# Kernel tuning notes

Measured on AMD Instinct MI355X. Metric: run time of the kernel, lower is better.

Reference implementation:

```python
import jax, jax.numpy as jnp
import numpy as np

NODE_CNT = 1_000_000
EMBED_DIM = 64
B = 4096
N0, N1 = 10, 25          # neighbor_cnt_list = [10, 25]
H0, H1 = 128, 128        # hidden_dim_list = [128, 128]


def setup_inputs() -> dict:
    key = jax.random.key(0)
    k_in, k_n0, k_n1, k_emb, k_w1, k_w0, k_b0 = jax.random.split(key, 7)
    inputs = jax.random.randint(k_in, (B,), 0, NODE_CNT, dtype=jnp.int32)
    neigh0 = jax.random.randint(k_n0, (B, N0), 0, NODE_CNT, dtype=jnp.int32)
    neigh1 = jax.random.randint(k_n1, (B, N0, N1), 0, NODE_CNT, dtype=jnp.int32)
    # learned parameters
    embed_table = jax.random.normal(k_emb, (NODE_CNT + 1, EMBED_DIM), dtype=jnp.float32) * 0.05
    # fc1: deepest layer, linear, no bias: (embed + mean-agg embed) -> H1
    W1 = jax.random.normal(k_w1, (2 * EMBED_DIM, H1), dtype=jnp.float32) * (1.0 / np.sqrt(2 * EMBED_DIM))
    # fc0: output layer, sigmoid + bias: (embed + mean-agg h1) -> H0
    W0 = jax.random.normal(k_w0, (EMBED_DIM + H1, H0), dtype=jnp.float32) * (1.0 / np.sqrt(EMBED_DIM + H1))
    b0 = jnp.zeros((H0,), dtype=jnp.float32)
    return {"inputs": inputs, "neigh0": neigh0, "neigh1": neigh1,
            "embed_table": embed_table, "W1": W1, "W0": W0, "b0": b0}


def reference(inputs, neigh0, neigh1, embed_table, W1, W0, b0):
    # ---- deepest level (k = 1): raw embedding gather + mean aggregate ----
    e_nn = embed_table[neigh1]                    # [B, N0, N1, D] irregular gather
    agg1 = jnp.mean(e_nn, axis=2)                 # [B, N0, D]
    e_n = embed_table[neigh0]                     # [B, N0, D]
    # fc1: linear, no bias, no activation
    h1 = jnp.concatenate([e_n, agg1], axis=-1) @ W1   # [B, N0, H1]
    # ---- level k = 0: aggregate layer-1 vectors of sampled neighbors ----
    agg0 = jnp.mean(h1, axis=1)                   # [B, H1]
    e_v = embed_table[inputs]                     # [B, D]
    # fc0: dense with bias + sigmoid
    h0 = jax.nn.sigmoid(jnp.concatenate([e_v, agg0], axis=-1) @ W0 + b0)  # [B, H0]
    return h0
```

## Files before the change

kernel.cpp:

```cpp
#include <hip/hip_runtime.h>
#include <math.h>


constexpr int D   = 64;
constexpr int N0  = 10;
constexpr int N1  = 25;
constexpr int NN  = N0 * N1;
constexpr int H1  = 128;
constexpr int H0  = 128;
constexpr int K0  = D + H1;
constexpr int BPB = 2;
constexpr int NT  = 256;

__global__ __launch_bounds__(NT, 8) void sage_fused(
    const int*   __restrict__ inputs,
    const int*   __restrict__ neigh0,
    const int*   __restrict__ neigh1,
    const float* __restrict__ embed,
    const float* __restrict__ W1,
    const float* __restrict__ W0,
    const float* __restrict__ b0,
    float*       __restrict__ out)
{
    __shared__ int   s_idx1[BPB * NN];
    __shared__ int   s_idx0[BPB * N0];
    __shared__ int   s_in[BPB];
    __shared__ float part_nn[16][D];
    __shared__ float part_en[16][D];
    __shared__ float xbar[BPB][2 * D];
    __shared__ float x0s[BPB][K0];
    __shared__ float p2[2][BPB][H1];

    const int t     = threadIdx.x;
    const int bbase = blockIdx.x * BPB;

    for (int i = t; i < BPB * NN; i += NT) s_idx1[i] = neigh1[bbase * NN + i];
    if (t < BPB * N0) s_idx0[t] = neigh0[bbase * N0 + t];
    if (t < BPB)      s_in[t]   = inputs[bbase + t];
    __syncthreads();

    const int c4lane = t & 15;
    const int s      = t >> 4;
    const int r      = s & (BPB - 1);
    const int ss     = s >> 1;
    const int cOff   = c4lane * 4;

    float4 sum_nn = make_float4(0.f, 0.f, 0.f, 0.f);
    #pragma unroll 4
    for (int i = ss; i < NN; i += 16 / BPB) {
        const int idx = s_idx1[r * NN + i];
        const float4 v = *(const float4*)(embed + (size_t)idx * D + cOff);
        sum_nn.x += v.x; sum_nn.y += v.y; sum_nn.z += v.z; sum_nn.w += v.w;
    }
    float4 sum_en = make_float4(0.f, 0.f, 0.f, 0.f);
    #pragma unroll
    for (int i = ss; i < N0; i += 16 / BPB) {
        const int idx = s_idx0[r * N0 + i];
        const float4 v = *(const float4*)(embed + (size_t)idx * D + cOff);
        sum_en.x += v.x; sum_en.y += v.y; sum_en.z += v.z; sum_en.w += v.w;
    }
    if (ss == 0) {
        const int idx = s_in[r];
        const float4 v = *(const float4*)(embed + (size_t)idx * D + cOff);
        *(float4*)&x0s[r][cOff] = v;
    }
    *(float4*)&part_nn[s][cOff] = sum_nn;
    *(float4*)&part_en[s][cOff] = sum_en;
    __syncthreads();

    if (t < BPB * D) {
        const int rr = t >> 6;
        const int c  = t & 63;
        float snn = 0.f, sen = 0.f;
        #pragma unroll
        for (int q = 0; q < 16 / BPB; ++q) {
            snn += part_nn[rr + BPB * q][c];
            sen += part_en[rr + BPB * q][c];
        }
        xbar[rr][c]     = sen * (1.0f / N0);
        xbar[rr][D + c] = snn * (1.0f / NN);
    }
    __syncthreads();

    const int j    = t & 127;
    const int half = t >> 7;
    {
        float acc[BPB];
        #pragma unroll
        for (int r2 = 0; r2 < BPB; ++r2) acc[r2] = 0.f;
        const int kbase = half * 64;
        #pragma unroll 4
        for (int k4 = 0; k4 < 16; ++k4) {
            const int k = kbase + k4 * 4;
            float4 xv[BPB];
            #pragma unroll
            for (int r2 = 0; r2 < BPB; ++r2)
                xv[r2] = *(const float4*)&xbar[r2][k];
            const float wa = W1[(k + 0) * H1 + j];
            const float wb = W1[(k + 1) * H1 + j];
            const float wc = W1[(k + 2) * H1 + j];
            const float wd = W1[(k + 3) * H1 + j];
            #pragma unroll
            for (int r2 = 0; r2 < BPB; ++r2)
                acc[r2] += xv[r2].x * wa + xv[r2].y * wb + xv[r2].z * wc + xv[r2].w * wd;
        }
        #pragma unroll
        for (int r2 = 0; r2 < BPB; ++r2) p2[half][r2][j] = acc[r2];
    }
    __syncthreads();
    for (int idx = t; idx < BPB * H1; idx += NT) {
        const int rr = idx >> 7, jj = idx & 127;
        x0s[rr][D + jj] = p2[0][rr][jj] + p2[1][rr][jj];
    }
    __syncthreads();

    {
        float acc[BPB];
        #pragma unroll
        for (int r2 = 0; r2 < BPB; ++r2) acc[r2] = 0.f;
        const int kbase = half * 96;
        #pragma unroll 4
        for (int k4 = 0; k4 < 24; ++k4) {
            const int k = kbase + k4 * 4;
            float4 xv[BPB];
            #pragma unroll
            for (int r2 = 0; r2 < BPB; ++r2)
                xv[r2] = *(const float4*)&x0s[r2][k];
            const float wa = W0[(k + 0) * H0 + j];
            const float wb = W0[(k + 1) * H0 + j];
            const float wc = W0[(k + 2) * H0 + j];
            const float wd = W0[(k + 3) * H0 + j];
            #pragma unroll
            for (int r2 = 0; r2 < BPB; ++r2)
                acc[r2] += xv[r2].x * wa + xv[r2].y * wb + xv[r2].z * wc + xv[r2].w * wd;
        }
        #pragma unroll
        for (int r2 = 0; r2 < BPB; ++r2) p2[half][r2][j] = acc[r2];
    }
    __syncthreads();
    for (int idx = t; idx < BPB * H0; idx += NT) {
        const int rr = idx >> 7, jj = idx & 127;
        const float v = p2[0][rr][jj] + p2[1][rr][jj] + b0[jj];
        out[(size_t)(bbase + rr) * H0 + jj] = 1.0f / (1.0f + __expf(-v));
    }
}

extern "C" void kernel_launch(void* const* d_in, const int* in_sizes, int n_in,
                              void* d_out, int out_size, void* d_ws, size_t ws_size,
                              hipStream_t stream) {
    const int*   inputs = (const int*)  d_in[0];
    const int*   neigh0 = (const int*)  d_in[1];
    const int*   neigh1 = (const int*)  d_in[2];
    const float* embed  = (const float*)d_in[3];
    const float* W1     = (const float*)d_in[4];
    const float* W0     = (const float*)d_in[5];
    const float* b0     = (const float*)d_in[6];
    float*       out    = (float*)d_out;

    const int B = in_sizes[0];
    const int nblocks = B / BPB;
    sage_fused<<<dim3(nblocks), dim3(NT), 0, stream>>>(
        inputs, neigh0, neigh1, embed, W1, W0, b0, out);
}
```

Measured before the change: 359.2 us.

## Process one batch row per block with 4-way independent gather accumulators

Switches from two batch rows per block to one, so each block of 256 threads gathers the 250 second-hop neighbor rows of a single node with all 16 row-groups. The gather loop is restructured to issue four independent float4 loads per iteration into separate accumulators, raising memory-level parallelism for the random embedding gather. Launch bounds drop from 8 to 4 waves-hint and the grid doubles, while the W1/W0 weights are now read twice as often per output row because weight reuse across two rows is lost.

```diff
diff --git a/kernel.cpp b/kernel.cpp
--- a/kernel.cpp
+++ b/kernel.cpp
@@ -8,11 +8,9 @@
 constexpr int NN  = N0 * N1;
 constexpr int H1  = 128;
 constexpr int H0  = 128;
-constexpr int K0  = D + H1;
-constexpr int BPB = 2;
 constexpr int NT  = 256;
 
-__global__ __launch_bounds__(NT, 8) void sage_fused(
+__global__ __launch_bounds__(NT, 4) void sage_fused(
     const int*   __restrict__ inputs,
     const int*   __restrict__ neigh0,
     const int*   __restrict__ neigh1,
@@ -22,126 +20,114 @@
     const float* __restrict__ b0,
     float*       __restrict__ out)
 {
-    __shared__ int   s_idx1[BPB * NN];
-    __shared__ int   s_idx0[BPB * N0];
-    __shared__ int   s_in[BPB];
+    __shared__ int   s_idx1[NN];
+    __shared__ int   s_idx0[N0];
+    __shared__ int   s_in;
     __shared__ float part_nn[16][D];
-    __shared__ float part_en[16][D];
-    __shared__ float xbar[BPB][2 * D];
-    __shared__ float x0s[BPB][K0];
-    __shared__ float p2[2][BPB][H1];
+    __shared__ float part_en[N0][D];
+    __shared__ float xbar[2 * D];
+    __shared__ float x0s[D + H1];
+    __shared__ float p2[2][H1];
 
-    const int t     = threadIdx.x;
-    const int bbase = blockIdx.x * BPB;
+    const int t = threadIdx.x;
+    const int b = blockIdx.x;
 
-    for (int i = t; i < BPB * NN; i += NT) s_idx1[i] = neigh1[bbase * NN + i];
-    if (t < BPB * N0) s_idx0[t] = neigh0[bbase * N0 + t];
-    if (t < BPB)      s_in[t]   = inputs[bbase + t];
+    if (t < NN)      s_idx1[t] = neigh1[b * NN + t];
+    if (t < N0)      s_idx0[t] = neigh0[b * N0 + t];
+    if (t == 0)      s_in      = inputs[b];
     __syncthreads();
 
-    const int c4lane = t & 15;
-    const int s      = t >> 4;
-    const int r      = s & (BPB - 1);
-    const int ss     = s >> 1;
-    const int cOff   = c4lane * 4;
+    const int c4   = t & 15;
+    const int s    = t >> 4;
+    const int cOff = c4 * 4;
 
-    float4 sum_nn = make_float4(0.f, 0.f, 0.f, 0.f);
-    #pragma unroll 4
-    for (int i = ss; i < NN; i += 16 / BPB) {
-        const int idx = s_idx1[r * NN + i];
-        const float4 v = *(const float4*)(embed + (size_t)idx * D + cOff);
-        sum_nn.x += v.x; sum_nn.y += v.y; sum_nn.z += v.z; sum_nn.w += v.w;
+    float4 a0 = make_float4(0,0,0,0), a1 = make_float4(0,0,0,0);
+    float4 a2 = make_float4(0,0,0,0), a3 = make_float4(0,0,0,0);
+    int i = s;
+    #pragma unroll 1
+    for (; i + 48 < NN; i += 64) {
+        const int i0 = s_idx1[i];
+        const int i1 = s_idx1[i + 16];
+        const int i2 = s_idx1[i + 32];
+        const int i3 = s_idx1[i + 48];
+        const float4 v0 = *(const float4*)(embed + (size_t)i0 * D + cOff);
+        const float4 v1 = *(const float4*)(embed + (size_t)i1 * D + cOff);
+        const float4 v2 = *(const float4*)(embed + (size_t)i2 * D + cOff);
+        const float4 v3 = *(const float4*)(embed + (size_t)i3 * D + cOff);
+        a0.x += v0.x; a0.y += v0.y; a0.z += v0.z; a0.w += v0.w;
+        a1.x += v1.x; a1.y += v1.y; a1.z += v1.z; a1.w += v1.w;
+        a2.x += v2.x; a2.y += v2.y; a2.z += v2.z; a2.w += v2.w;
+        a3.x += v3.x; a3.y += v3.y; a3.z += v3.z; a3.w += v3.w;
     }
-    float4 sum_en = make_float4(0.f, 0.f, 0.f, 0.f);
-    #pragma unroll
-    for (int i = ss; i < N0; i += 16 / BPB) {
-        const int idx = s_idx0[r * N0 + i];
-        const float4 v = *(const float4*)(embed + (size_t)idx * D + cOff);
-        sum_en.x += v.x; sum_en.y += v.y; sum_en.z += v.z; sum_en.w += v.w;
+    #pragma unroll 1
+    for (; i < NN; i += 16) {
+        const float4 v = *(const float4*)(embed + (size_t)s_idx1[i] * D + cOff);
+        a0.x += v.x; a0.y += v.y; a0.z += v.z; a0.w += v.w;
     }
-    if (ss == 0) {
-        const int idx = s_in[r];
-        const float4 v = *(const float4*)(embed + (size_t)idx * D + cOff);
-        *(float4*)&x0s[r][cOff] = v;
+    a0.x += a1.x + a2.x + a3.x;  a0.y += a1.y + a2.y + a3.y;
+    a0.z += a1.z + a2.z + a3.z;  a0.w += a1.w + a2.w + a3.w;
+    *(float4*)&part_nn[s][cOff] = a0;
+
+    if (s < N0) {
+        const float4 v = *(const float4*)(embed + (size_t)s_idx0[s] * D + cOff);
+        *(float4*)&part_en[s][cOff] = v;
     }
-    *(float4*)&part_nn[s][cOff] = sum_nn;
-    *(float4*)&part_en[s][cOff] = sum_en;
+    if (t < 16) {
+        const float4 v = *(const float4*)(embed + (size_t)s_in * D + t * 4);
+        *(float4*)&x0s[t * 4] = v;
+    }
     __syncthreads();
 
-    if (t < BPB * D) {
-        const int rr = t >> 6;
-        const int c  = t & 63;
-        float snn = 0.f, sen = 0.f;
+    if (t < D) {
+        float snn = 0.f;
         #pragma unroll
-        for (int q = 0; q < 16 / BPB; ++q) {
-            snn += part_nn[rr + BPB * q][c];
-            sen += part_en[rr + BPB * q][c];
-        }
-        xbar[rr][c]     = sen * (1.0f / N0);
-        xbar[rr][D + c] = snn * (1.0f / NN);
+        for (int q = 0; q < 16; ++q) snn += part_nn[q][t];
+        float sen = 0.f;
+        #pragma unroll
+        for (int q = 0; q < N0; ++q) sen += part_en[q][t];
+        xbar[t]     = sen * (1.0f / N0);
+        xbar[D + t] = snn * (1.0f / NN);
     }
     __syncthreads();
 
     const int j    = t & 127;
     const int half = t >> 7;
     {
-        float acc[BPB];
-        #pragma unroll
-        for (int r2 = 0; r2 < BPB; ++r2) acc[r2] = 0.f;
+        float acc = 0.f;
         const int kbase = half * 64;
         #pragma unroll 4
         for (int k4 = 0; k4 < 16; ++k4) {
             const int k = kbase + k4 * 4;
-            float4 xv[BPB];
-            #pragma unroll
-            for (int r2 = 0; r2 < BPB; ++r2)
-                xv[r2] = *(const float4*)&xbar[r2][k];
-            const float wa = W1[(k + 0) * H1 + j];
-            const float wb = W1[(k + 1) * H1 + j];
-            const float wc = W1[(k + 2) * H1 + j];
-            const float wd = W1[(k + 3) * H1 + j];
-            #pragma unroll
-            for (int r2 = 0; r2 < BPB; ++r2)
-                acc[r2] += xv[r2].x * wa + xv[r2].y * wb + xv[r2].z * wc + xv[r2].w * wd;
+            const float4 xv = *(const float4*)&xbar[k];
+            acc += xv.x * W1[(k + 0) * H1 + j];
+            acc += xv.y * W1[(k + 1) * H1 + j];
+            acc += xv.z * W1[(k + 2) * H1 + j];
+            acc += xv.w * W1[(k + 3) * H1 + j];
         }
-        #pragma unroll
-        for (int r2 = 0; r2 < BPB; ++r2) p2[half][r2][j] = acc[r2];
+        p2[half][j] = acc;
     }
     __syncthreads();
-    for (int idx = t; idx < BPB * H1; idx += NT) {
-        const int rr = idx >> 7, jj = idx & 127;
-        x0s[rr][D + jj] = p2[0][rr][jj] + p2[1][rr][jj];
-    }
+    if (t < H1) x0s[D + t] = p2[0][t] + p2[1][t];
     __syncthreads();
 
     {
-        float acc[BPB];
-        #pragma unroll
-        for (int r2 = 0; r2 < BPB; ++r2) acc[r2] = 0.f;
+        float acc = 0.f;
         const int kbase = half * 96;
         #pragma unroll 4
         for (int k4 = 0; k4 < 24; ++k4) {
             const int k = kbase + k4 * 4;
-            float4 xv[BPB];
-            #pragma unroll
-            for (int r2 = 0; r2 < BPB; ++r2)
-                xv[r2] = *(const float4*)&x0s[r2][k];
-            const float wa = W0[(k + 0) * H0 + j];
-            const float wb = W0[(k + 1) * H0 + j];
-            const float wc = W0[(k + 2) * H0 + j];
-            const float wd = W0[(k + 3) * H0 + j];
-            #pragma unroll
-            for (int r2 = 0; r2 < BPB; ++r2)
-                acc[r2] += xv[r2].x * wa + xv[r2].y * wb + xv[r2].z * wc + xv[r2].w * wd;
+            const float4 xv = *(const float4*)&x0s[k];
+            acc += xv.x * W0[(k + 0) * H0 + j];
+            acc += xv.y * W0[(k + 1) * H0 + j];
+            acc += xv.z * W0[(k + 2) * H0 + j];
+            acc += xv.w * W0[(k + 3) * H0 + j];
         }
-        #pragma unroll
-        for (int r2 = 0; r2 < BPB; ++r2) p2[half][r2][j] = acc[r2];
+        p2[half][j] = acc;
     }
     __syncthreads();
-    for (int idx = t; idx < BPB * H0; idx += NT) {
-        const int rr = idx >> 7, jj = idx & 127;
-        const float v = p2[0][rr][jj] + p2[1][rr][jj] + b0[jj];
-        out[(size_t)(bbase + rr) * H0 + jj] = 1.0f / (1.0f + __expf(-v));
+    if (t < H0) {
+        const float v = p2[0][t] + p2[1][t] + b0[t];
+        out[(size_t)b * H0 + t] = 1.0f / (1.0f + __expf(-v));
     }
 }
 
@@ -158,7 +144,6 @@
     float*       out    = (float*)d_out;
 
     const int B = in_sizes[0];
-    const int nblocks = B / BPB;
-    sage_fused<<<dim3(nblocks), dim3(NT), 0, stream>>>(
+    sage_fused<<<dim3(B), dim3(NT), 0, stream>>>(
         inputs, neigh0, neigh1, embed, W1, W0, b0, out);
 }
```

After: 362.2 us (median of 2 runs). Within noise of the previous version (+0.8%).
